# Kernel tuning notes

Measured on AMD Instinct MI355X. Metric: run time of the kernel, lower is better.

Reference implementation:

```python
import jax, jax.numpy as jnp
import numpy as np

EPS = 1e-5  # torch InstanceNorm1d default eps
H = 64      # band_features


def instance_norm(x):
    # x: [B, T, F]; torch applies InstanceNorm1d on [B, F, T], i.e. normalize
    # over the length axis T per (batch, channel). No affine params.
    mu = jnp.mean(x, axis=1, keepdims=True)
    var = jnp.var(x, axis=1, keepdims=True)  # biased variance, as torch
    return (x - mu) * jax.lax.rsqrt(var + EPS)


def lstm_layer(x, Wih, Whh, bih, bhh):
    # x: [B, T, D_in]; Wih: [4H, D_in]; Whh: [4H, H]; gate order i,f,g,o (torch)
    B, T, _ = x.shape
    xp = jnp.einsum('btd,gd->btg', x, Wih) + bih + bhh   # [B, T, 4H]
    xp = jnp.swapaxes(xp, 0, 1)                          # [T, B, 4H]

    def step(carry, xt):
        h, c = carry
        gates = xt + h @ Whh.T                           # [B, 4H]
        i, f, g, o = jnp.split(gates, 4, axis=-1)
        c = jax.nn.sigmoid(f) * c + jax.nn.sigmoid(i) * jnp.tanh(g)
        h = jax.nn.sigmoid(o) * jnp.tanh(c)
        return (h, c), h

    h0 = jnp.zeros((B, H), x.dtype)
    _, hs = jax.lax.scan(step, (h0, h0), xp)             # hs: [T, B, H]
    return jnp.swapaxes(hs, 0, 1)                        # [B, T, H]


def setup_inputs() -> dict:
    key = jax.random.key(0)
    ks = jax.random.split(key, 12)
    B, T = 64, 4096
    bound = 1.0 / np.sqrt(H)  # torch LSTM/Linear default init scale

    def u(k, shape):
        return jax.random.uniform(k, shape, jnp.float32, -bound, bound)

    return {
        'x': jax.random.normal(ks[0], (B, T, H), jnp.float32),
        'Wih0': u(ks[1], (4 * H, H)), 'Whh0': u(ks[2], (4 * H, H)),
        'bih0': u(ks[3], (4 * H,)),   'bhh0': u(ks[4], (4 * H,)),
        'Wih1': u(ks[5], (4 * H, H)), 'Whh1': u(ks[6], (4 * H, H)),
        'bih1': u(ks[7], (4 * H,)),   'bhh1': u(ks[8], (4 * H,)),
        'Wfc': u(ks[9], (H, H)),      'bfc': u(ks[10], (H,)),
    }


def reference(x, Wih0, Whh0, bih0, bhh0, Wih1, Whh1, bih1, bhh1, Wfc, bfc):
    out = instance_norm(x)
    out = lstm_layer(out, Wih0, Whh0, bih0, bhh0)
    out = lstm_layer(out, Wih1, Whh1, bih1, bhh1)
    out = jnp.einsum('bth,oh->bto', out, Wfc) + bfc
    return out + x
```

## Files before the change

kernel.cpp:

```cpp
#include <hip/hip_runtime.h>
#include <cstddef>
#include <cstdint>

#define BB 64
#define TT 4096
#define HD 64
#define FP 72

typedef _Float16 f16;
typedef _Float16 f16x8 __attribute__((ext_vector_type(8)));
typedef _Float16 f16x4 __attribute__((ext_vector_type(4)));
typedef _Float16 f16x2 __attribute__((ext_vector_type(2)));
typedef float f32x4 __attribute__((ext_vector_type(4)));
typedef float v2f __attribute__((ext_vector_type(2)));

__device__ __forceinline__ void bar_lgkm() {
    asm volatile("s_waitcnt lgkmcnt(0)\n\ts_barrier" ::: "memory");
}

__global__ __launch_bounds__(256) void stats_part(const float* __restrict__ x,
                                                  float* __restrict__ part) {
    const int b = blockIdx.x >> 2, seg = blockIdx.x & 3;
    const int f = threadIdx.x & 63, grp = threadIdx.x >> 6;
    const float* xb = x + (size_t)b * TT * HD + (size_t)seg * (TT / 4) * HD;
    float s = 0.f, s2 = 0.f;
    for (int t = grp; t < TT / 4; t += 4) {
        float v = xb[t * HD + f];
        s += v;
        s2 = fmaf(v, v, s2);
    }
    __shared__ float ls[4][64];
    __shared__ float ls2[4][64];
    ls[grp][f] = s;
    ls2[grp][f] = s2;
    __syncthreads();
    if (threadIdx.x < 64) {
        float ss = 0.f, ss2 = 0.f;
#pragma unroll
        for (int i = 0; i < 4; ++i) { ss += ls[i][f]; ss2 += ls2[i][f]; }
        part[blockIdx.x * HD + f] = ss;
        part[256 * HD + blockIdx.x * HD + f] = ss2;
    }
}

__global__ __launch_bounds__(64) void stats_fin(const float* __restrict__ part,
                                                float* __restrict__ stats) {
    const int b = blockIdx.x, f = threadIdx.x;
    float s = 0.f, s2 = 0.f;
#pragma unroll
    for (int seg = 0; seg < 4; ++seg) {
        s += part[(b * 4 + seg) * HD + f];
        s2 += part[256 * HD + (b * 4 + seg) * HD + f];
    }
    float mu = s * (1.0f / TT);
    float var = s2 * (1.0f / TT) - mu * mu;
    stats[b * HD + f] = mu;
    stats[BB * HD + b * HD + f] = rsqrtf(var + 1e-5f);
}

__global__ __launch_bounds__(512, 2) void rnn_mfma(
    const float* __restrict__ x,
    const float* __restrict__ Wih0, const float* __restrict__ Whh0,
    const float* __restrict__ bih0, const float* __restrict__ bhh0,
    const float* __restrict__ Wih1, const float* __restrict__ Whh1,
    const float* __restrict__ bih1, const float* __restrict__ bhh1,
    const float* __restrict__ stats,
    float* __restrict__ h1out) {
    const int blk = blockIdx.x;
    const int tid = threadIdx.x;
    const int lane = tid & 63;
    const int wid = tid >> 6;
    const bool L1w = (wid < 4);
    const int wq = wid & 3;
    const int ln15 = lane & 15;
    const int l16 = lane >> 4;

    __shared__ __align__(16) f16 hT0[2][16 * FP];
    __shared__ __align__(16) f16 hT1[16][16 * FP];
    __shared__ __align__(16) f16 xnb[2][8][16 * FP];

    const float* WA = L1w ? Wih1 : Whh0;
    const float* WBm = L1w ? Whh1 : Wih0;
    uint32_t aA[4][2][4], aB[4][2][4];
#pragma unroll
    for (int i = 0; i < 4; ++i) {
        const int row = 64 * i + 16 * wq + ln15;
#pragma unroll
        for (int kt = 0; kt < 2; ++kt) {
            const int fb = 32 * kt + 8 * l16;
            const float4 a0 = *(const float4*)&WA[row * HD + fb];
            const float4 a1 = *(const float4*)&WA[row * HD + fb + 4];
            const float4 b0 = *(const float4*)&WBm[row * HD + fb];
            const float4 b1 = *(const float4*)&WBm[row * HD + fb + 4];
            f16x8 ha = {(f16)a0.x, (f16)a0.y, (f16)a0.z, (f16)a0.w,
                        (f16)a1.x, (f16)a1.y, (f16)a1.z, (f16)a1.w};
            f16x8 hb = {(f16)b0.x, (f16)b0.y, (f16)b0.z, (f16)b0.w,
                        (f16)b1.x, (f16)b1.y, (f16)b1.z, (f16)b1.w};
            uint4 ua = __builtin_bit_cast(uint4, ha);
            uint4 ub = __builtin_bit_cast(uint4, hb);
            asm volatile("v_accvgpr_write_b32 %0, %1" : "=a"(aA[i][kt][0]) : "v"(ua.x));
            asm volatile("v_accvgpr_write_b32 %0, %1" : "=a"(aA[i][kt][1]) : "v"(ua.y));
            asm volatile("v_accvgpr_write_b32 %0, %1" : "=a"(aA[i][kt][2]) : "v"(ua.z));
            asm volatile("v_accvgpr_write_b32 %0, %1" : "=a"(aA[i][kt][3]) : "v"(ua.w));
            asm volatile("v_accvgpr_write_b32 %0, %1" : "=a"(aB[i][kt][0]) : "v"(ub.x));
            asm volatile("v_accvgpr_write_b32 %0, %1" : "=a"(aB[i][kt][1]) : "v"(ub.y));
            asm volatile("v_accvgpr_write_b32 %0, %1" : "=a"(aB[i][kt][2]) : "v"(ub.z));
            asm volatile("v_accvgpr_write_b32 %0, %1" : "=a"(aB[i][kt][3]) : "v"(ub.w));
        }
    }
    f16x8 wAf[4][2], wBf[4][2];
#pragma unroll
    for (int i = 0; i < 4; ++i)
#pragma unroll
        for (int kt = 0; kt < 2; ++kt) {
            uint4 ua = {aA[i][kt][0], aA[i][kt][1], aA[i][kt][2], aA[i][kt][3]};
            uint4 ub = {aB[i][kt][0], aB[i][kt][1], aB[i][kt][2], aB[i][kt][3]};
            wAf[i][kt] = __builtin_bit_cast(f16x8, ua);
            wBf[i][kt] = __builtin_bit_cast(f16x8, ub);
        }

    const float* bi = L1w ? bih1 : bih0;
    const float* bh = L1w ? bhh1 : bhh0;
    f32x4 bias[4];
#pragma unroll
    for (int i = 0; i < 4; ++i)
#pragma unroll
        for (int r = 0; r < 4; ++r) {
            const int row = 64 * i + 16 * wq + 4 * l16 + r;
            bias[i][r] = bi[row] + bh[row];
        }

    const int sb = tid >> 5;
    const int f2 = (tid & 31) * 2;
    const size_t gb = (size_t)blk * 16 + sb;
    const float mux = stats[gb * HD + f2];
    const float muy = stats[gb * HD + f2 + 1];
    const float rsx = stats[(size_t)BB * HD + gb * HD + f2];
    const float rsy = stats[(size_t)BB * HD + gb * HD + f2 + 1];
    const v2f aa = {rsx, rsy};
    const v2f bbv = {-mux * rsx, -muy * rsy};
    const float* xrow = x + gb * TT * HD;
    float* orow = h1out + gb * TT * HD;

    for (int i = tid; i < 2 * 16 * FP / 2; i += 512) ((unsigned*)hT0)[i] = 0u;
    for (int i = tid; i < 16 * 16 * FP / 2; i += 512) ((unsigned*)hT1)[i] = 0u;

    v2f xr[8];
#pragma unroll
    for (int tau = 0; tau < 8; ++tau) {
        v2f v = *(const v2f*)&xrow[(size_t)tau * HD + f2];
        f16x2 xh;
        xh.x = (f16)fmaf(v.x, aa.x, bbv.x);
        xh.y = (f16)fmaf(v.y, aa.y, bbv.y);
        *(f16x2*)&xnb[0][tau][sb * FP + f2] = xh;
    }
#pragma unroll
    for (int tau = 0; tau < 8; ++tau)
        xr[tau] = *(const v2f*)&xrow[(size_t)(8 + tau) * HD + f2];

    v2f cstp[2] = {{0.f, 0.f}, {0.f, 0.f}};

    auto PHASE = [&](const f16* src1, const f16* src2, f16* dest) {
        f16x8 B1k0 = *(const f16x8*)&src1[ln15 * FP + 8 * l16];
        f16x8 B1k1 = *(const f16x8*)&src1[ln15 * FP + 32 + 8 * l16];
        f16x8 B2k0 = *(const f16x8*)&src2[ln15 * FP + 8 * l16];
        f16x8 B2k1 = *(const f16x8*)&src2[ln15 * FP + 32 + 8 * l16];
        f32x4 acc[4];
#pragma unroll
        for (int i = 0; i < 4; ++i) {
            acc[i] = bias[i];
            acc[i] = __builtin_amdgcn_mfma_f32_16x16x32_f16(wAf[i][0], B1k0, acc[i], 0, 0, 0);
            acc[i] = __builtin_amdgcn_mfma_f32_16x16x32_f16(wAf[i][1], B1k1, acc[i], 0, 0, 0);
            acc[i] = __builtin_amdgcn_mfma_f32_16x16x32_f16(wBf[i][0], B2k0, acc[i], 0, 0, 0);
            acc[i] = __builtin_amdgcn_mfma_f32_16x16x32_f16(wBf[i][1], B2k1, acc[i], 0, 0, 0);
        }
        uint32_t hw[2];
#pragma unroll
        for (int rp = 0; rp < 2; ++rp) {
            v2f gi = {acc[0][2 * rp], acc[0][2 * rp + 1]};
            v2f gf = {acc[1][2 * rp], acc[1][2 * rp + 1]};
            v2f gg = {acc[2][2 * rp], acc[2][2 * rp + 1]};
            v2f go = {acc[3][2 * rp], acc[3][2 * rp + 1]};
            v2f ti = gi * -1.44269504f;
            v2f tf = gf * -1.44269504f;
            v2f tg = gg * 2.88539008f;
            v2f to = go * -1.44269504f;
            v2f emi = {__builtin_amdgcn_exp2f(ti.x), __builtin_amdgcn_exp2f(ti.y)};
            v2f emf = {__builtin_amdgcn_exp2f(tf.x), __builtin_amdgcn_exp2f(tf.y)};
            v2f eg2 = {__builtin_amdgcn_exp2f(tg.x), __builtin_amdgcn_exp2f(tg.y)};
            v2f emo = {__builtin_amdgcn_exp2f(to.x), __builtin_amdgcn_exp2f(to.y)};
            v2f dig = (emi + 1.0f) * (eg2 + 1.0f);
            v2f rig = {__builtin_amdgcn_rcpf(dig.x), __builtin_amdgcn_rcpf(dig.y)};
            v2f ig = (eg2 - 1.0f) * rig;
            v2f dnf = emf + 1.0f;
            v2f fg2 = {__builtin_amdgcn_rcpf(dnf.x), __builtin_amdgcn_rcpf(dnf.y)};
            v2f c = fg2 * cstp[rp] + ig;
            cstp[rp] = c;
            v2f tc2 = c * 2.88539008f;
            v2f ec2 = {__builtin_amdgcn_exp2f(tc2.x), __builtin_amdgcn_exp2f(tc2.y)};
            v2f dno = (emo + 1.0f) * (ec2 + 1.0f);
            v2f rno = {__builtin_amdgcn_rcpf(dno.x), __builtin_amdgcn_rcpf(dno.y)};
            v2f h = (ec2 - 1.0f) * rno;
            f16x2 hh;
            hh.x = (f16)h.x;
            hh.y = (f16)h.y;
            hw[rp] = __builtin_bit_cast(uint32_t, hh);
        }
        uint2 hu = {hw[0], hw[1]};
        *(f16x4*)&dest[ln15 * FP + 16 * wq + 4 * l16] = __builtin_bit_cast(f16x4, hu);
    };

    bar_lgkm();
    if (!L1w) PHASE(&hT0[1][0], &xnb[0][0][0], &hT0[0][0]);
    bar_lgkm();

    for (int tb = 0; tb < TT; tb += 16) {
#pragma unroll
        for (int k = 0; k < 16; ++k) {
            {
                const f16* src1 = &hT0[k & 1][0];
                const f16* src2 = L1w ? &hT1[(k + 15) & 15][0]
                                      : &xnb[((k + 1) >> 3) & 1][(k + 1) & 7][0];
                f16* dest = L1w ? &hT1[k & 15][0] : &hT0[(k + 1) & 1][0];
                PHASE(src1, src2, dest);
            }
            if (tb > 0 || k >= 2) {
                f16x2 hh = *(const f16x2*)&hT1[(k + 14) & 15][sb * FP + f2];
                v2f o = {(float)hh.x, (float)hh.y};
                *(v2f*)&orow[(size_t)(tb + k - 2) * HD + f2] = o;
            }
            {
                const int tc = k & 7;
                if (k < 8 || tb < TT - 16) {
                    const int bufw = (k < 8) ? 1 : 0;
                    v2f v = xr[tc];
                    f16x2 xh;
                    xh.x = (f16)fmaf(v.x, aa.x, bbv.x);
                    xh.y = (f16)fmaf(v.y, aa.y, bbv.y);
                    *(f16x2*)&xnb[bufw][tc][sb * FP + f2] = xh;
                }
                if (tb < TT - 16) {
                    xr[tc] = *(const v2f*)&xrow[(size_t)(tb + 16 + k) * HD + f2];
                }
            }
            bar_lgkm();
        }
    }
    {
        f16x2 h14 = *(const f16x2*)&hT1[14][sb * FP + f2];
        v2f o14 = {(float)h14.x, (float)h14.y};
        *(v2f*)&orow[(size_t)(TT - 2) * HD + f2] = o14;
        f16x2 h15 = *(const f16x2*)&hT1[15][sb * FP + f2];
        v2f o15 = {(float)h15.x, (float)h15.y};
        *(v2f*)&orow[(size_t)(TT - 1) * HD + f2] = o15;
    }
}

__global__ __launch_bounds__(256) void fc_res(float* __restrict__ hout,
                                              const float* __restrict__ x,
                                              const float* __restrict__ Wfc,
                                              const float* __restrict__ bfc) {
    __shared__ __align__(16) float wfc_lds[HD * HD];
    __shared__ float bfc_lds[HD];
    const int tid = threadIdx.x;
#pragma unroll
    for (int i = 0; i < 4; ++i)
        ((float4*)wfc_lds)[tid + 256 * i] = ((const float4*)Wfc)[tid + 256 * i];
    if (tid < HD) bfc_lds[tid] = bfc[tid];

    const size_t row = (size_t)blockIdx.x * 256 + tid;
    float hr[HD];
    {
        const float4* hp = (const float4*)(hout + row * HD);
#pragma unroll
        for (int i = 0; i < 16; ++i) {
            float4 v = hp[i];
            hr[4 * i] = v.x; hr[4 * i + 1] = v.y;
            hr[4 * i + 2] = v.z; hr[4 * i + 3] = v.w;
        }
    }
    __syncthreads();

    const float4* xp = (const float4*)(x + row * HD);
    float4* op = (float4*)(hout + row * HD);
    for (int j4 = 0; j4 < 16; ++j4) {
        float s0 = 0.f, s1 = 0.f, s2 = 0.f, s3 = 0.f;
        const float* w0 = &wfc_lds[(4 * j4 + 0) * HD];
        const float* w1 = &wfc_lds[(4 * j4 + 1) * HD];
        const float* w2 = &wfc_lds[(4 * j4 + 2) * HD];
        const float* w3 = &wfc_lds[(4 * j4 + 3) * HD];
#pragma unroll
        for (int k = 0; k < HD; ++k) {
            s0 = fmaf(w0[k], hr[k], s0);
            s1 = fmaf(w1[k], hr[k], s1);
            s2 = fmaf(w2[k], hr[k], s2);
            s3 = fmaf(w3[k], hr[k], s3);
        }
        float4 xv = xp[j4];
        float4 o;
        o.x = s0 + bfc_lds[4 * j4 + 0] + xv.x;
        o.y = s1 + bfc_lds[4 * j4 + 1] + xv.y;
        o.z = s2 + bfc_lds[4 * j4 + 2] + xv.z;
        o.w = s3 + bfc_lds[4 * j4 + 3] + xv.w;
        op[j4] = o;
    }
}

extern "C" void kernel_launch(void* const* d_in, const int* in_sizes, int n_in,
                              void* d_out, int out_size, void* d_ws, size_t ws_size,
                              hipStream_t stream) {
    const float* x    = (const float*)d_in[0];
    const float* Wih0 = (const float*)d_in[1];
    const float* Whh0 = (const float*)d_in[2];
    const float* bih0 = (const float*)d_in[3];
    const float* bhh0 = (const float*)d_in[4];
    const float* Wih1 = (const float*)d_in[5];
    const float* Whh1 = (const float*)d_in[6];
    const float* bih1 = (const float*)d_in[7];
    const float* bhh1 = (const float*)d_in[8];
    const float* Wfc  = (const float*)d_in[9];
    const float* bfc  = (const float*)d_in[10];

    float* part  = (float*)d_ws;
    float* stats = part + 2 * 256 * HD;
    float* out   = (float*)d_out;

    stats_part<<<256, 256, 0, stream>>>(x, part);
    stats_fin<<<64, 64, 0, stream>>>(part, stats);
    rnn_mfma<<<4, 512, 0, stream>>>(x, Wih0, Whh0, bih0, bhh0,
                                    Wih1, Whh1, bih1, bhh1, stats, out);
    fc_res<<<1024, 256, 0, stream>>>(out, x, Wfc, bfc);
}
```

Measured before the change: 3.296 ms.

## Interleave two batch groups per block and halve the RNN grid

```diff
diff --git a/kernel.cpp b/kernel.cpp
--- a/kernel.cpp
+++ b/kernel.cpp
@@ -6,6 +6,7 @@
 #define TT 4096
 #define HD 64
 #define FP 72
+#define SZ (16 * FP)
 
 typedef _Float16 f16;
 typedef _Float16 f16x8 __attribute__((ext_vector_type(8)));
@@ -75,9 +76,9 @@
     const int ln15 = lane & 15;
     const int l16 = lane >> 4;
 
-    __shared__ __align__(16) f16 hT0[2][16 * FP];
-    __shared__ __align__(16) f16 hT1[16][16 * FP];
-    __shared__ __align__(16) f16 xnb[2][8][16 * FP];
+    __shared__ __align__(16) f16 hT0[2][2 * SZ];
+    __shared__ __align__(16) f16 hT1[2][8 * SZ];
+    __shared__ __align__(16) f16 xnb[2][2][8 * SZ];
 
     const float* WA = L1w ? Wih1 : Whh0;
     const float* WBm = L1w ? Whh1 : Wih0;
@@ -132,35 +133,41 @@
 
     const int sb = tid >> 5;
     const int f2 = (tid & 31) * 2;
-    const size_t gb = (size_t)blk * 16 + sb;
-    const float mux = stats[gb * HD + f2];
-    const float muy = stats[gb * HD + f2 + 1];
-    const float rsx = stats[(size_t)BB * HD + gb * HD + f2];
-    const float rsy = stats[(size_t)BB * HD + gb * HD + f2 + 1];
-    const v2f aa = {rsx, rsy};
-    const v2f bbv = {-mux * rsx, -muy * rsy};
-    const float* xrow = x + gb * TT * HD;
-    float* orow = h1out + gb * TT * HD;
-
-    for (int i = tid; i < 2 * 16 * FP / 2; i += 512) ((unsigned*)hT0)[i] = 0u;
-    for (int i = tid; i < 16 * 16 * FP / 2; i += 512) ((unsigned*)hT1)[i] = 0u;
-
-    v2f xr[8];
+    const size_t gbA = (size_t)blk * 32 + sb;
+    const size_t gbB = gbA + 16;
+    const v2f aaA = {stats[BB * HD + gbA * HD + f2], stats[BB * HD + gbA * HD + f2 + 1]};
+    const v2f aaB = {stats[BB * HD + gbB * HD + f2], stats[BB * HD + gbB * HD + f2 + 1]};
+    const v2f bbA = {-stats[gbA * HD + f2] * aaA.x, -stats[gbA * HD + f2 + 1] * aaA.y};
+    const v2f bbB = {-stats[gbB * HD + f2] * aaB.x, -stats[gbB * HD + f2 + 1] * aaB.y};
+    const float* xrowA = x + gbA * TT * HD;
+    const float* xrowB = x + gbB * TT * HD;
+    float* orowA = h1out + gbA * TT * HD;
+    float* orowB = h1out + gbB * TT * HD;
+
+    for (int i = tid; i < 2 * 2 * SZ / 2; i += 512) ((unsigned*)hT0)[i] = 0u;
+    for (int i = tid; i < 2 * 8 * SZ / 2; i += 512) ((unsigned*)hT1)[i] = 0u;
+
+    v2f xrA[8], xrB[8];
 #pragma unroll
     for (int tau = 0; tau < 8; ++tau) {
-        v2f v = *(const v2f*)&xrow[(size_t)tau * HD + f2];
-        f16x2 xh;
-        xh.x = (f16)fmaf(v.x, aa.x, bbv.x);
-        xh.y = (f16)fmaf(v.y, aa.y, bbv.y);
-        *(f16x2*)&xnb[0][tau][sb * FP + f2] = xh;
-    }
-#pragma unroll
-    for (int tau = 0; tau < 8; ++tau)
-        xr[tau] = *(const v2f*)&xrow[(size_t)(8 + tau) * HD + f2];
-
-    v2f cstp[2] = {{0.f, 0.f}, {0.f, 0.f}};
-
-    auto PHASE = [&](const f16* src1, const f16* src2, f16* dest) {
+        v2f vA = *(const v2f*)&xrowA[(size_t)tau * HD + f2];
+        v2f vB = *(const v2f*)&xrowB[(size_t)tau * HD + f2];
+        f16x2 hA, hB;
+        hA.x = (f16)fmaf(vA.x, aaA.x, bbA.x); hA.y = (f16)fmaf(vA.y, aaA.y, bbA.y);
+        hB.x = (f16)fmaf(vB.x, aaB.x, bbB.x); hB.y = (f16)fmaf(vB.y, aaB.y, bbB.y);
+        *(f16x2*)&xnb[0][0][tau * SZ + sb * FP + f2] = hA;
+        *(f16x2*)&xnb[1][0][tau * SZ + sb * FP + f2] = hB;
+    }
+#pragma unroll
+    for (int tau = 0; tau < 8; ++tau) {
+        xrA[tau] = *(const v2f*)&xrowA[(size_t)(8 + tau) * HD + f2];
+        xrB[tau] = *(const v2f*)&xrowB[(size_t)(8 + tau) * HD + f2];
+    }
+
+    v2f cstA[2] = {{0.f, 0.f}, {0.f, 0.f}};
+    v2f cstB[2] = {{0.f, 0.f}, {0.f, 0.f}};
+
+    auto PHASE = [&](v2f* cstp, const f16* src1, const f16* src2, f16* dest) {
         f16x8 B1k0 = *(const f16x8*)&src1[ln15 * FP + 8 * l16];
         f16x8 B1k1 = *(const f16x8*)&src1[ln15 * FP + 32 + 8 * l16];
         f16x8 B2k0 = *(const f16x8*)&src2[ln15 * FP + 8 * l16];
@@ -210,49 +217,74 @@
         *(f16x4*)&dest[ln15 * FP + 16 * wq + 4 * l16] = __builtin_bit_cast(f16x4, hu);
     };
 
+    auto STEP = [&](int n2, int tb, v2f* cstg, v2f* xrg, f16* hT0g, f16* hT1g,
+                    f16* xnbP, f16* xnbQ, v2f aa, v2f bbv,
+                    const float* xrowg, float* __restrict__ orowg,
+                    bool doLoad, bool doXnb) {
+        const f16* src1 = hT0g + (n2 & 1) * SZ;
+        const f16* src2 = L1w ? hT1g + ((n2 + 7) & 7) * SZ
+                              : (n2 < 7 ? xnbP + (n2 + 1) * SZ : xnbQ);
+        f16* dest = L1w ? hT1g + n2 * SZ : hT0g + ((n2 + 1) & 1) * SZ;
+        PHASE(cstg, src1, src2, dest);
+        const int k = tb + n2;
+        if (tb > 0 || n2 >= 2) {
+            f16x2 hh = *(const f16x2*)&hT1g[((n2 + 6) & 7) * SZ + sb * FP + f2];
+            v2f o = {(float)hh.x, (float)hh.y};
+            *(v2f*)&orowg[(size_t)(k - 2) * HD + f2] = o;
+        }
+        if (doXnb) {
+            v2f v = xrg[n2];
+            f16x2 xh;
+            xh.x = (f16)fmaf(v.x, aa.x, bbv.x);
+            xh.y = (f16)fmaf(v.y, aa.y, bbv.y);
+            *(f16x2*)&xnbQ[n2 * SZ + sb * FP + f2] = xh;
+        }
+        if (doLoad) {
+            xrg[n2] = *(const v2f*)&xrowg[(size_t)(k + 16) * HD + f2];
+        }
+    };
+
     bar_lgkm();
-    if (!L1w) PHASE(&hT0[1][0], &xnb[0][0][0], &hT0[0][0]);
+    if (!L1w) {
+        PHASE(cstA, hT0[0] + SZ, &xnb[0][0][0], hT0[0]);
+        PHASE(cstB, hT0[1] + SZ, &xnb[1][0][0], hT0[1]);
+    }
     bar_lgkm();
 
-    for (int tb = 0; tb < TT; tb += 16) {
-#pragma unroll
-        for (int k = 0; k < 16; ++k) {
-            {
-                const f16* src1 = &hT0[k & 1][0];
-                const f16* src2 = L1w ? &hT1[(k + 15) & 15][0]
-                                      : &xnb[((k + 1) >> 3) & 1][(k + 1) & 7][0];
-                f16* dest = L1w ? &hT1[k & 15][0] : &hT0[(k + 1) & 1][0];
-                PHASE(src1, src2, dest);
-            }
-            if (tb > 0 || k >= 2) {
-                f16x2 hh = *(const f16x2*)&hT1[(k + 14) & 15][sb * FP + f2];
-                v2f o = {(float)hh.x, (float)hh.y};
-                *(v2f*)&orow[(size_t)(tb + k - 2) * HD + f2] = o;
-            }
-            {
-                const int tc = k & 7;
-                if (k < 8 || tb < TT - 16) {
-                    const int bufw = (k < 8) ? 1 : 0;
-                    v2f v = xr[tc];
-                    f16x2 xh;
-                    xh.x = (f16)fmaf(v.x, aa.x, bbv.x);
-                    xh.y = (f16)fmaf(v.y, aa.y, bbv.y);
-                    *(f16x2*)&xnb[bufw][tc][sb * FP + f2] = xh;
-                }
-                if (tb < TT - 16) {
-                    xr[tc] = *(const v2f*)&xrow[(size_t)(tb + 16 + k) * HD + f2];
-                }
-            }
+    for (int tb = 0; tb < TT; tb += 8) {
+        const int P = (tb >> 3) & 1;
+        f16* xnbPA = xnb[0][P];
+        f16* xnbQA = xnb[0][P ^ 1];
+        f16* xnbPB = xnb[1][P];
+        f16* xnbQB = xnb[1][P ^ 1];
+        const bool doLoad = (tb < TT - 16);
+        const bool doXnb = (tb < TT - 8);
+#pragma unroll
+        for (int n = 0; n < 16; ++n) {
+            const int n2 = n >> 1;
+            if ((n & 1) == 0)
+                STEP(n2, tb, cstA, xrA, hT0[0], hT1[0], xnbPA, xnbQA,
+                     aaA, bbA, xrowA, orowA, doLoad, doXnb);
+            else
+                STEP(n2, tb, cstB, xrB, hT0[1], hT1[1], xnbPB, xnbQB,
+                     aaB, bbB, xrowB, orowB, doLoad, doXnb);
             bar_lgkm();
         }
     }
     {
-        f16x2 h14 = *(const f16x2*)&hT1[14][sb * FP + f2];
-        v2f o14 = {(float)h14.x, (float)h14.y};
-        *(v2f*)&orow[(size_t)(TT - 2) * HD + f2] = o14;
-        f16x2 h15 = *(const f16x2*)&hT1[15][sb * FP + f2];
-        v2f o15 = {(float)h15.x, (float)h15.y};
-        *(v2f*)&orow[(size_t)(TT - 1) * HD + f2] = o15;
+        f16x2 a6 = *(const f16x2*)&hT1[0][6 * SZ + sb * FP + f2];
+        f16x2 a7 = *(const f16x2*)&hT1[0][7 * SZ + sb * FP + f2];
+        v2f o;
+        o = (v2f){(float)a6.x, (float)a6.y};
+        *(v2f*)&orowA[(size_t)(TT - 2) * HD + f2] = o;
+        o = (v2f){(float)a7.x, (float)a7.y};
+        *(v2f*)&orowA[(size_t)(TT - 1) * HD + f2] = o;
+        f16x2 b6 = *(const f16x2*)&hT1[1][6 * SZ + sb * FP + f2];
+        f16x2 b7 = *(const f16x2*)&hT1[1][7 * SZ + sb * FP + f2];
+        o = (v2f){(float)b6.x, (float)b6.y};
+        *(v2f*)&orowB[(size_t)(TT - 2) * HD + f2] = o;
+        o = (v2f){(float)b7.x, (float)b7.y};
+        *(v2f*)&orowB[(size_t)(TT - 1) * HD + f2] = o;
     }
 }
 
@@ -327,7 +359,7 @@
 
     stats_part<<<256, 256, 0, stream>>>(x, part);
     stats_fin<<<64, 64, 0, stream>>>(part, stats);
-    rnn_mfma<<<4, 512, 0, stream>>>(x, Wih0, Whh0, bih0, bhh0,
+    rnn_mfma<<<2, 512, 0, stream>>>(x, Wih0, Whh0, bih0, bhh0,
                                     Wih1, Whh1, bih1, bhh1, stats, out);
     fc_res<<<1024, 256, 0, stream>>>(out, x, Wfc, bfc);
 }
```

Measured after the change: 6.505 ms. 97.3% more time.

## Fuse both LSTM layers into each wave, halving block size to four waves

Applied to the files above, without the earlier changes.

```diff
diff --git a/kernel.cpp b/kernel.cpp
--- a/kernel.cpp
+++ b/kernel.cpp
@@ -58,7 +58,7 @@
     stats[BB * HD + b * HD + f] = rsqrtf(var + 1e-5f);
 }
 
-__global__ __launch_bounds__(512, 2) void rnn_mfma(
+__global__ __launch_bounds__(256, 1) void rnn_mfma(
     const float* __restrict__ x,
     const float* __restrict__ Wih0, const float* __restrict__ Whh0,
     const float* __restrict__ bih0, const float* __restrict__ bhh0,
@@ -69,9 +69,7 @@
     const int blk = blockIdx.x;
     const int tid = threadIdx.x;
     const int lane = tid & 63;
-    const int wid = tid >> 6;
-    const bool L1w = (wid < 4);
-    const int wq = wid & 3;
+    const int wq = tid >> 6;
     const int ln15 = lane & 15;
     const int l16 = lane >> 4;
 
@@ -79,101 +77,92 @@
     __shared__ __align__(16) f16 hT1[16][16 * FP];
     __shared__ __align__(16) f16 xnb[2][8][16 * FP];
 
-    const float* WA = L1w ? Wih1 : Whh0;
-    const float* WBm = L1w ? Whh1 : Wih0;
-    uint32_t aA[4][2][4], aB[4][2][4];
-#pragma unroll
-    for (int i = 0; i < 4; ++i) {
-        const int row = 64 * i + 16 * wq + ln15;
+    uint32_t ag[2][2][4][2][4];
+#pragma unroll
+    for (int L = 0; L < 2; ++L) {
+        const float* WA = L ? Wih1 : Whh0;
+        const float* WBm = L ? Whh1 : Wih0;
+#pragma unroll
+        for (int i = 0; i < 4; ++i) {
+            const int row = 64 * i + 16 * wq + ln15;
+#pragma unroll
+            for (int kt = 0; kt < 2; ++kt) {
+                const int fb = 32 * kt + 8 * l16;
+                const float4 a0 = *(const float4*)&WA[row * HD + fb];
+                const float4 a1 = *(const float4*)&WA[row * HD + fb + 4];
+                const float4 b0 = *(const float4*)&WBm[row * HD + fb];
+                const float4 b1 = *(const float4*)&WBm[row * HD + fb + 4];
+                f16x8 ha = {(f16)a0.x, (f16)a0.y, (f16)a0.z, (f16)a0.w,
+                            (f16)a1.x, (f16)a1.y, (f16)a1.z, (f16)a1.w};
+                f16x8 hb = {(f16)b0.x, (f16)b0.y, (f16)b0.z, (f16)b0.w,
+                            (f16)b1.x, (f16)b1.y, (f16)b1.z, (f16)b1.w};
+                uint4 ua = __builtin_bit_cast(uint4, ha);
+                uint4 ub = __builtin_bit_cast(uint4, hb);
+                asm volatile("v_accvgpr_write_b32 %0, %1" : "=a"(ag[L][0][i][kt][0]) : "v"(ua.x));
+                asm volatile("v_accvgpr_write_b32 %0, %1" : "=a"(ag[L][0][i][kt][1]) : "v"(ua.y));
+                asm volatile("v_accvgpr_write_b32 %0, %1" : "=a"(ag[L][0][i][kt][2]) : "v"(ua.z));
+                asm volatile("v_accvgpr_write_b32 %0, %1" : "=a"(ag[L][0][i][kt][3]) : "v"(ua.w));
+                asm volatile("v_accvgpr_write_b32 %0, %1" : "=a"(ag[L][1][i][kt][0]) : "v"(ub.x));
+                asm volatile("v_accvgpr_write_b32 %0, %1" : "=a"(ag[L][1][i][kt][1]) : "v"(ub.y));
+                asm volatile("v_accvgpr_write_b32 %0, %1" : "=a"(ag[L][1][i][kt][2]) : "v"(ub.z));
+                asm volatile("v_accvgpr_write_b32 %0, %1" : "=a"(ag[L][1][i][kt][3]) : "v"(ub.w));
+            }
+        }
+    }
+    f16x8 wA1[4][2], wB1[4][2], wA0[4][2], wB0[4][2];
+#pragma unroll
+    for (int i = 0; i < 4; ++i)
 #pragma unroll
         for (int kt = 0; kt < 2; ++kt) {
-            const int fb = 32 * kt + 8 * l16;
-            const float4 a0 = *(const float4*)&WA[row * HD + fb];
-            const float4 a1 = *(const float4*)&WA[row * HD + fb + 4];
-            const float4 b0 = *(const float4*)&WBm[row * HD + fb];
-            const float4 b1 = *(const float4*)&WBm[row * HD + fb + 4];
-            f16x8 ha = {(f16)a0.x, (f16)a0.y, (f16)a0.z, (f16)a0.w,
-                        (f16)a1.x, (f16)a1.y, (f16)a1.z, (f16)a1.w};
-            f16x8 hb = {(f16)b0.x, (f16)b0.y, (f16)b0.z, (f16)b0.w,
-                        (f16)b1.x, (f16)b1.y, (f16)b1.z, (f16)b1.w};
-            uint4 ua = __builtin_bit_cast(uint4, ha);
-            uint4 ub = __builtin_bit_cast(uint4, hb);
-            asm volatile("v_accvgpr_write_b32 %0, %1" : "=a"(aA[i][kt][0]) : "v"(ua.x));
-            asm volatile("v_accvgpr_write_b32 %0, %1" : "=a"(aA[i][kt][1]) : "v"(ua.y));
-            asm volatile("v_accvgpr_write_b32 %0, %1" : "=a"(aA[i][kt][2]) : "v"(ua.z));
-            asm volatile("v_accvgpr_write_b32 %0, %1" : "=a"(aA[i][kt][3]) : "v"(ua.w));
-            asm volatile("v_accvgpr_write_b32 %0, %1" : "=a"(aB[i][kt][0]) : "v"(ub.x));
-            asm volatile("v_accvgpr_write_b32 %0, %1" : "=a"(aB[i][kt][1]) : "v"(ub.y));
-            asm volatile("v_accvgpr_write_b32 %0, %1" : "=a"(aB[i][kt][2]) : "v"(ub.z));
-            asm volatile("v_accvgpr_write_b32 %0, %1" : "=a"(aB[i][kt][3]) : "v"(ub.w));
-        }
-    }
-    f16x8 wAf[4][2], wBf[4][2];
-#pragma unroll
-    for (int i = 0; i < 4; ++i)
-#pragma unroll
-        for (int kt = 0; kt < 2; ++kt) {
-            uint4 ua = {aA[i][kt][0], aA[i][kt][1], aA[i][kt][2], aA[i][kt][3]};
-            uint4 ub = {aB[i][kt][0], aB[i][kt][1], aB[i][kt][2], aB[i][kt][3]};
-            wAf[i][kt] = __builtin_bit_cast(f16x8, ua);
-            wBf[i][kt] = __builtin_bit_cast(f16x8, ub);
-        }
-
-    const float* bi = L1w ? bih1 : bih0;
-    const float* bh = L1w ? bhh1 : bhh0;
-    f32x4 bias[4];
+            uint4 u10 = {ag[1][0][i][kt][0], ag[1][0][i][kt][1], ag[1][0][i][kt][2], ag[1][0][i][kt][3]};
+            uint4 u11 = {ag[1][1][i][kt][0], ag[1][1][i][kt][1], ag[1][1][i][kt][2], ag[1][1][i][kt][3]};
+            uint4 u00 = {ag[0][0][i][kt][0], ag[0][0][i][kt][1], ag[0][0][i][kt][2], ag[0][0][i][kt][3]};
+            uint4 u01 = {ag[0][1][i][kt][0], ag[0][1][i][kt][1], ag[0][1][i][kt][2], ag[0][1][i][kt][3]};
+            wA1[i][kt] = __builtin_bit_cast(f16x8, u10);
+            wB1[i][kt] = __builtin_bit_cast(f16x8, u11);
+            wA0[i][kt] = __builtin_bit_cast(f16x8, u00);
+            wB0[i][kt] = __builtin_bit_cast(f16x8, u01);
+        }
+
+    f32x4 bias1[4], bias0[4];
 #pragma unroll
     for (int i = 0; i < 4; ++i)
 #pragma unroll
         for (int r = 0; r < 4; ++r) {
             const int row = 64 * i + 16 * wq + 4 * l16 + r;
-            bias[i][r] = bi[row] + bh[row];
-        }
-
-    const int sb = tid >> 5;
-    const int f2 = (tid & 31) * 2;
+            bias1[i][r] = bih1[row] + bhh1[row];
+            bias0[i][r] = bih0[row] + bhh0[row];
+        }
+
+    const int sb = tid >> 4;
+    const int fq = (tid & 15) * 4;
     const size_t gb = (size_t)blk * 16 + sb;
-    const float mux = stats[gb * HD + f2];
-    const float muy = stats[gb * HD + f2 + 1];
-    const float rsx = stats[(size_t)BB * HD + gb * HD + f2];
-    const float rsy = stats[(size_t)BB * HD + gb * HD + f2 + 1];
-    const v2f aa = {rsx, rsy};
-    const v2f bbv = {-mux * rsx, -muy * rsy};
+    const float4 mu4 = *(const float4*)&stats[gb * HD + fq];
+    const float4 rs4 = *(const float4*)&stats[(size_t)BB * HD + gb * HD + fq];
+    const float4 aa4 = rs4;
+    const float4 bb4 = {-mu4.x * rs4.x, -mu4.y * rs4.y, -mu4.z * rs4.z, -mu4.w * rs4.w};
     const float* xrow = x + gb * TT * HD;
     float* orow = h1out + gb * TT * HD;
 
-    for (int i = tid; i < 2 * 16 * FP / 2; i += 512) ((unsigned*)hT0)[i] = 0u;
-    for (int i = tid; i < 16 * 16 * FP / 2; i += 512) ((unsigned*)hT1)[i] = 0u;
-
-    v2f xr[8];
+    for (int i = tid; i < 2 * 16 * FP / 2; i += 256) ((unsigned*)hT0)[i] = 0u;
+    for (int i = tid; i < 16 * 16 * FP / 2; i += 256) ((unsigned*)hT1)[i] = 0u;
+
+    float4 xr[8];
 #pragma unroll
     for (int tau = 0; tau < 8; ++tau) {
-        v2f v = *(const v2f*)&xrow[(size_t)tau * HD + f2];
-        f16x2 xh;
-        xh.x = (f16)fmaf(v.x, aa.x, bbv.x);
-        xh.y = (f16)fmaf(v.y, aa.y, bbv.y);
-        *(f16x2*)&xnb[0][tau][sb * FP + f2] = xh;
+        float4 v = *(const float4*)&xrow[(size_t)tau * HD + fq];
+        f16x4 h4 = {(f16)fmaf(v.x, aa4.x, bb4.x), (f16)fmaf(v.y, aa4.y, bb4.y),
+                    (f16)fmaf(v.z, aa4.z, bb4.z), (f16)fmaf(v.w, aa4.w, bb4.w)};
+        *(f16x4*)&xnb[0][tau][sb * FP + fq] = h4;
     }
 #pragma unroll
     for (int tau = 0; tau < 8; ++tau)
-        xr[tau] = *(const v2f*)&xrow[(size_t)(8 + tau) * HD + f2];
-
-    v2f cstp[2] = {{0.f, 0.f}, {0.f, 0.f}};
-
-    auto PHASE = [&](const f16* src1, const f16* src2, f16* dest) {
-        f16x8 B1k0 = *(const f16x8*)&src1[ln15 * FP + 8 * l16];
-        f16x8 B1k1 = *(const f16x8*)&src1[ln15 * FP + 32 + 8 * l16];
-        f16x8 B2k0 = *(const f16x8*)&src2[ln15 * FP + 8 * l16];
-        f16x8 B2k1 = *(const f16x8*)&src2[ln15 * FP + 32 + 8 * l16];
-        f32x4 acc[4];
-#pragma unroll
-        for (int i = 0; i < 4; ++i) {
-            acc[i] = bias[i];
-            acc[i] = __builtin_amdgcn_mfma_f32_16x16x32_f16(wAf[i][0], B1k0, acc[i], 0, 0, 0);
-            acc[i] = __builtin_amdgcn_mfma_f32_16x16x32_f16(wAf[i][1], B1k1, acc[i], 0, 0, 0);
-            acc[i] = __builtin_amdgcn_mfma_f32_16x16x32_f16(wBf[i][0], B2k0, acc[i], 0, 0, 0);
-            acc[i] = __builtin_amdgcn_mfma_f32_16x16x32_f16(wBf[i][1], B2k1, acc[i], 0, 0, 0);
-        }
+        xr[tau] = *(const float4*)&xrow[(size_t)(8 + tau) * HD + fq];
+
+    v2f cst1[2] = {{0.f, 0.f}, {0.f, 0.f}};
+    v2f cst0[2] = {{0.f, 0.f}, {0.f, 0.f}};
+
+    auto ACT = [&](f32x4* acc, v2f* cstp) -> f16x4 {
         uint32_t hw[2];
 #pragma unroll
         for (int rp = 0; rp < 2; ++rp) {
@@ -207,52 +196,98 @@
             hw[rp] = __builtin_bit_cast(uint32_t, hh);
         }
         uint2 hu = {hw[0], hw[1]};
-        *(f16x4*)&dest[ln15 * FP + 16 * wq + 4 * l16] = __builtin_bit_cast(f16x4, hu);
+        return __builtin_bit_cast(f16x4, hu);
     };
 
+    auto PHASE2 = [&](const f16* s1, const f16* s2, const f16* s3,
+                      f16* d1, f16* d0) {
+        f16x8 B1k0 = *(const f16x8*)&s1[ln15 * FP + 8 * l16];
+        f16x8 B1k1 = *(const f16x8*)&s1[ln15 * FP + 32 + 8 * l16];
+        f16x8 B2k0 = *(const f16x8*)&s2[ln15 * FP + 8 * l16];
+        f16x8 B2k1 = *(const f16x8*)&s2[ln15 * FP + 32 + 8 * l16];
+        f16x8 B3k0 = *(const f16x8*)&s3[ln15 * FP + 8 * l16];
+        f16x8 B3k1 = *(const f16x8*)&s3[ln15 * FP + 32 + 8 * l16];
+        f32x4 acc1[4], acc0[4];
+#pragma unroll
+        for (int i = 0; i < 4; ++i) {
+            acc1[i] = bias1[i];
+            acc1[i] = __builtin_amdgcn_mfma_f32_16x16x32_f16(wA1[i][0], B1k0, acc1[i], 0, 0, 0);
+            acc1[i] = __builtin_amdgcn_mfma_f32_16x16x32_f16(wA1[i][1], B1k1, acc1[i], 0, 0, 0);
+            acc1[i] = __builtin_amdgcn_mfma_f32_16x16x32_f16(wB1[i][0], B2k0, acc1[i], 0, 0, 0);
+            acc1[i] = __builtin_amdgcn_mfma_f32_16x16x32_f16(wB1[i][1], B2k1, acc1[i], 0, 0, 0);
+            acc0[i] = bias0[i];
+            acc0[i] = __builtin_amdgcn_mfma_f32_16x16x32_f16(wA0[i][0], B1k0, acc0[i], 0, 0, 0);
+            acc0[i] = __builtin_amdgcn_mfma_f32_16x16x32_f16(wA0[i][1], B1k1, acc0[i], 0, 0, 0);
+            acc0[i] = __builtin_amdgcn_mfma_f32_16x16x32_f16(wB0[i][0], B3k0, acc0[i], 0, 0, 0);
+            acc0[i] = __builtin_amdgcn_mfma_f32_16x16x32_f16(wB0[i][1], B3k1, acc0[i], 0, 0, 0);
+        }
+        f16x4 h1v = ACT(acc1, cst1);
+        f16x4 h0v = ACT(acc0, cst0);
+        *(f16x4*)&d1[ln15 * FP + 16 * wq + 4 * l16] = h1v;
+        *(f16x4*)&d0[ln15 * FP + 16 * wq + 4 * l16] = h0v;
+    };
+
     bar_lgkm();
-    if (!L1w) PHASE(&hT0[1][0], &xnb[0][0][0], &hT0[0][0]);
+    {
+        const f16* s1 = &hT0[1][0];
+        const f16* s3 = &xnb[0][0][0];
+        f16x8 B1k0 = *(const f16x8*)&s1[ln15 * FP + 8 * l16];
+        f16x8 B1k1 = *(const f16x8*)&s1[ln15 * FP + 32 + 8 * l16];
+        f16x8 B3k0 = *(const f16x8*)&s3[ln15 * FP + 8 * l16];
+        f16x8 B3k1 = *(const f16x8*)&s3[ln15 * FP + 32 + 8 * l16];
+        f32x4 acc0[4];
+#pragma unroll
+        for (int i = 0; i < 4; ++i) {
+            acc0[i] = bias0[i];
+            acc0[i] = __builtin_amdgcn_mfma_f32_16x16x32_f16(wA0[i][0], B1k0, acc0[i], 0, 0, 0);
+            acc0[i] = __builtin_amdgcn_mfma_f32_16x16x32_f16(wA0[i][1], B1k1, acc0[i], 0, 0, 0);
+            acc0[i] = __builtin_amdgcn_mfma_f32_16x16x32_f16(wB0[i][0], B3k0, acc0[i], 0, 0, 0);
+            acc0[i] = __builtin_amdgcn_mfma_f32_16x16x32_f16(wB0[i][1], B3k1, acc0[i], 0, 0, 0);
+        }
+        f16x4 h0v = ACT(acc0, cst0);
+        *(f16x4*)&hT0[0][ln15 * FP + 16 * wq + 4 * l16] = h0v;
+    }
     bar_lgkm();
 
     for (int tb = 0; tb < TT; tb += 16) {
 #pragma unroll
         for (int k = 0; k < 16; ++k) {
             {
-                const f16* src1 = &hT0[k & 1][0];
-                const f16* src2 = L1w ? &hT1[(k + 15) & 15][0]
-                                      : &xnb[((k + 1) >> 3) & 1][(k + 1) & 7][0];
-                f16* dest = L1w ? &hT1[k & 15][0] : &hT0[(k + 1) & 1][0];
-                PHASE(src1, src2, dest);
+                const f16* s1 = &hT0[k & 1][0];
+                const f16* s2 = &hT1[(k + 15) & 15][0];
+                const f16* s3 = &xnb[((k + 1) >> 3) & 1][(k + 1) & 7][0];
+                f16* d1 = &hT1[k & 15][0];
+                f16* d0 = &hT0[(k + 1) & 1][0];
+                PHASE2(s1, s2, s3, d1, d0);
             }
             if (tb > 0 || k >= 2) {
-                f16x2 hh = *(const f16x2*)&hT1[(k + 14) & 15][sb * FP + f2];
-                v2f o = {(float)hh.x, (float)hh.y};
-                *(v2f*)&orow[(size_t)(tb + k - 2) * HD + f2] = o;
+                f16x4 hh = *(const f16x4*)&hT1[(k + 14) & 15][sb * FP + fq];
+                float4 o = {(float)hh[0], (float)hh[1], (float)hh[2], (float)hh[3]};
+                *(float4*)&orow[(size_t)(tb + k - 2) * HD + fq] = o;
             }
             {
                 const int tc = k & 7;
                 if (k < 8 || tb < TT - 16) {
                     const int bufw = (k < 8) ? 1 : 0;
-                    v2f v = xr[tc];
-                    f16x2 xh;
-                    xh.x = (f16)fmaf(v.x, aa.x, bbv.x);
-                    xh.y = (f16)fmaf(v.y, aa.y, bbv.y);
-                    *(f16x2*)&xnb[bufw][tc][sb * FP + f2] = xh;
+                    float4 v = xr[tc];
+                    f16x4 h4 = {(f16)fmaf(v.x, aa4.x, bb4.x), (f16)fmaf(v.y, aa4.y, bb4.y),
+                                (f16)fmaf(v.z, aa4.z, bb4.z), (f16)fmaf(v.w, aa4.w, bb4.w)};
+                    *(f16x4*)&xnb[bufw][tc][sb * FP + fq] = h4;
                 }
                 if (tb < TT - 16) {
-                    xr[tc] = *(const v2f*)&xrow[(size_t)(tb + 16 + k) * HD + f2];
+                    xr[tc] = *(const float4*)&xrow[(size_t)(tb + 16 + k) * HD + fq];
                 }
             }
             bar_lgkm();
         }
     }
     {
-        f16x2 h14 = *(const f16x2*)&hT1[14][sb * FP + f2];
-        v2f o14 = {(float)h14.x, (float)h14.y};
-        *(v2f*)&orow[(size_t)(TT - 2) * HD + f2] = o14;
-        f16x2 h15 = *(const f16x2*)&hT1[15][sb * FP + f2];
-        v2f o15 = {(float)h15.x, (float)h15.y};
-        *(v2f*)&orow[(size_t)(TT - 1) * HD + f2] = o15;
+        f16x4 h14 = *(const f16x4*)&hT1[14][sb * FP + fq];
+        float4 o14 = {(float)h14[0], (float)h14[1], (float)h14[2], (float)h14[3]};
+        *(float4*)&orow[(size_t)(TT - 2) * HD + fq] = o14;
+        f16x4 h15 = *(const f16x4*)&hT1[15][sb * FP + fq];
+        float4 o15 = {(float)h15[0], (float)h15[1], (float)h15[2], (float)h15[3]};
+        *(float4*)&orow[(size_t)(TT - 1) * HD + fq] = o15;
     }
 }
 
@@ -327,7 +362,7 @@
 
     stats_part<<<256, 256, 0, stream>>>(x, part);
     stats_fin<<<64, 64, 0, stream>>>(part, stats);
-    rnn_mfma<<<4, 512, 0, stream>>>(x, Wih0, Whh0, bih0, bhh0,
+    rnn_mfma<<<4, 256, 0, stream>>>(x, Wih0, Whh0, bih0, bhh0,
                                     Wih1, Whh1, bih1, bhh1, stats, out);
     fc_res<<<1024, 256, 0, stream>>>(out, x, Wfc, bfc);
 }
```

Result: slower. 3.478 ms (+5.5%).
